# Optimization experiments

Hardware: AMD Instinct MI355X
Metric: run time of the kernel (lower is better)

The kernel has to match this reference:

```python
import jax, jax.numpy as jnp
import numpy as np

N = 50000      # nodes
E = 800000     # edges (avg degree 16)
F_IN = 256
F_OUT = 256


def setup_inputs() -> dict:
    key = jax.random.key(0)
    ks = jax.random.split(key, 8)
    feature = jax.random.normal(ks[0], (N, F_IN), dtype=jnp.float32)
    e_w = jax.random.uniform(ks[1], (E, 1), dtype=jnp.float32)
    snorm_n = jnp.ones((N, 1), dtype=jnp.float32)
    snorm_e = jnp.ones((E, 1), dtype=jnp.float32)
    src = jax.random.randint(ks[2], (E,), 0, N, dtype=jnp.int32)
    dst = jax.random.randint(ks[3], (E,), 0, N, dtype=jnp.int32)
    scale = 1.0 / np.sqrt(F_IN)
    W_self = jax.random.normal(ks[4], (F_IN, F_OUT), dtype=jnp.float32) * scale
    W = jax.random.normal(ks[5], (F_IN, F_OUT), dtype=jnp.float32) * scale
    b = jax.random.normal(ks[6], (F_OUT,), dtype=jnp.float32) * scale
    return {"feature": feature, "e_w": e_w, "snorm_n": snorm_n,
            "snorm_e": snorm_e, "W_self": W_self, "W": W, "b": b,
            "src": src, "dst": dst}


def reference(feature, e_w, snorm_n, snorm_e, W_self, W, b, src, dst):
    n = feature.shape[0]
    ones_e = jnp.ones_like(src, dtype=feature.dtype)
    # self transform
    h_s = feature @ W_self                                   # [N, F_OUT]
    # source-side degree normalization: deg_out^{-1/2}
    out_deg = jnp.maximum(jax.ops.segment_sum(ones_e, src, num_segments=n), 1.0)
    feat = feature * (out_deg ** -0.5)[:, None]              # [N, F_IN]
    # message = h[src] * e_w, aggregated by sum into dst (u_mul_e + sum reduce)
    msgs = feat[src] * e_w                                   # [E, F_IN]
    agg = jax.ops.segment_sum(msgs, dst, num_segments=n)     # [N, F_IN]
    # neighbor transform + destination-side degree normalization
    h = agg @ W + b                                          # [N, F_OUT]
    in_deg = jnp.maximum(jax.ops.segment_sum(ones_e, dst, num_segments=n), 1.0)
    h = h * (in_deg ** -0.5)[:, None]
    return h_s + h, e_w
```

## Files before the change

### kernel.cpp

```cpp
#include <hip/hip_runtime.h>
#include <hip/hip_bf16.h>

#define N_NODES 50000
#define N_EDGES 800000
#define MP      50048
#define MAXDEG  64

#define EDGE_BLOCKS   3125
#define PREP_A_BLOCKS 12512
#define PREPW_BLOCKS  512

typedef __bf16 bf16x8_t __attribute__((ext_vector_type(8)));
typedef float  f32x4_t  __attribute__((ext_vector_type(4)));

__device__ __forceinline__ unsigned short f2bf(float x) {
  __hip_bfloat16 h = __float2bfloat16(x);
  return __builtin_bit_cast(unsigned short, h);
}

__global__ __launch_bounds__(256) void prep_fused(
    const float* __restrict__ feature, const float* __restrict__ Wself,
    const float* __restrict__ W, const float* __restrict__ e_w,
    const int* __restrict__ src, const int* __restrict__ dst,
    unsigned short* __restrict__ Abf, unsigned short* __restrict__ Bt,
    int* __restrict__ cnt_in, int* __restrict__ cnt_out,
    uint2* __restrict__ bucket, float* __restrict__ out1)
{
  const int b = blockIdx.x, tid = threadIdx.x;
  if (b < EDGE_BLOCKS) {
    int e = b * 256 + tid;
    if (e < N_EDGES) {
      int s = src[e];
      int d = dst[e];
      float w = e_w[e];
      out1[e] = w;
      atomicAdd(&cnt_out[s], 1);
      int p = atomicAdd(&cnt_in[d], 1);
      if (p < MAXDEG)
        bucket[(size_t)d * MAXDEG + p] = make_uint2(__float_as_uint(w), (unsigned)s);
    }
  } else if (b < EDGE_BLOCKS + PREP_A_BLOCKS) {
    int idx4 = (b - EDGE_BLOCKS) * 256 + tid;
    size_t base = (size_t)idx4 * 4;
    int row = (int)(base >> 8);
    ushort4 o;
    if (row < N_NODES) {
      const float4 v = *(const float4*)(feature + base);
      o.x = f2bf(v.x); o.y = f2bf(v.y); o.z = f2bf(v.z); o.w = f2bf(v.w);
    } else {
      o.x = o.y = o.z = o.w = 0;
    }
    *(ushort4*)(Abf + base) = o;
  } else {
    int idx = (b - (EDGE_BLOCKS + PREP_A_BLOCKS)) * 256 + tid;
    int n = idx >> 8, k = idx & 255;
    float v = (n < 256) ? Wself[k * 256 + n] : W[k * 256 + (n - 256)];
    Bt[idx] = f2bf(v);
  }
}

__global__ __launch_bounds__(256, 2) void gemm_kernel(
    const unsigned short* __restrict__ A,
    const unsigned short* __restrict__ Bt,
    const float* __restrict__ bias,
    const int* __restrict__ cnt_in,
    const int* __restrict__ cnt_out,
    float* __restrict__ out0,
    unsigned char* __restrict__ y8)
{
  __shared__ unsigned short As[128 * 32];
  __shared__ unsigned short Bs[256 * 32];
  const int tid  = threadIdx.x;
  const int lane = tid & 63;
  const int wave = tid >> 6;
  const int m0 = blockIdx.x * 128;
  const int n0 = blockIdx.y * 256;
  const int wm = (wave & 1) * 64;
  const int wn = (wave >> 1) * 128;
  const int fr = lane & 15;
  const int fk = (lane >> 4) * 8;
  const int srow  = lane >> 2;
  const int scolb = (lane & 3) * 8;

  f32x4_t acc[4][8] = {};

  for (int k0 = 0; k0 < 256; k0 += 32) {
#pragma unroll
    for (int j = 0; j < 2; ++j) {
      int rr = wave * 32 + j * 16;
      const unsigned short* ga = A + (size_t)(m0 + rr + srow) * 256 + (k0 + scolb);
      __builtin_amdgcn_global_load_lds((const __attribute__((address_space(1))) void*)ga,
                                       (__attribute__((address_space(3))) void*)&As[rr * 32],
                                       16, 0, 0);
    }
#pragma unroll
    for (int j = 0; j < 4; ++j) {
      int rr = wave * 64 + j * 16;
      const unsigned short* gb = Bt + (size_t)(n0 + rr + srow) * 256 + (k0 + scolb);
      __builtin_amdgcn_global_load_lds((const __attribute__((address_space(1))) void*)gb,
                                       (__attribute__((address_space(3))) void*)&Bs[rr * 32],
                                       16, 0, 0);
    }
    __syncthreads();

    bf16x8_t af[4], bfr[8];
#pragma unroll
    for (int i = 0; i < 4; ++i)
      af[i]  = *(const bf16x8_t*)&As[(wm + i * 16 + fr) * 32 + fk];
#pragma unroll
    for (int j = 0; j < 8; ++j)
      bfr[j] = *(const bf16x8_t*)&Bs[(wn + j * 16 + fr) * 32 + fk];
#pragma unroll
    for (int i = 0; i < 4; ++i)
#pragma unroll
      for (int j = 0; j < 8; ++j)
        acc[i][j] = __builtin_amdgcn_mfma_f32_16x16x32_bf16(af[i], bfr[j], acc[i][j], 0, 0, 0);
    __syncthreads();
  }

  if (blockIdx.y == 0) {
#pragma unroll
    for (int i = 0; i < 4; ++i) {
      int rowb = m0 + wm + i * 16 + (lane >> 4) * 4;
      float indv[4];
#pragma unroll
      for (int r = 0; r < 4; ++r) {
        int row = rowb + r;
        if (row < N_NODES) {
          int ci = cnt_in[row]; if (ci < 1) ci = 1;
          indv[r] = rsqrtf((float)ci);
        } else indv[r] = 0.f;
      }
#pragma unroll
      for (int j = 0; j < 8; ++j) {
        int col = wn + j * 16 + (lane & 15);
        float bc = bias[col];
#pragma unroll
        for (int r = 0; r < 4; ++r) {
          int row = rowb + r;
          if (row < N_NODES)
            out0[(size_t)row * 256 + col] = acc[i][j][r] + bc * indv[r];
        }
      }
    }
  } else {
#pragma unroll
    for (int i = 0; i < 4; ++i) {
      int rowb = m0 + wm + i * 16 + (lane >> 4) * 4;
      float odv[4];
#pragma unroll
      for (int r = 0; r < 4; ++r) {
        int row = rowb + r;
        if (row < N_NODES) {
          int co = cnt_out[row]; if (co < 1) co = 1;
          odv[r] = rsqrtf((float)co);
        } else odv[r] = 0.f;
      }
#pragma unroll
      for (int j = 0; j < 8; ++j) {
        int col = wn + j * 16 + (lane & 15);
#pragma unroll
        for (int r = 0; r < 4; ++r) {
          int row = rowb + r;
          if (row < N_NODES) {
            float ys = acc[i][j][r] * odv[r];
            unsigned int pk = (unsigned int)__builtin_amdgcn_cvt_pk_fp8_f32(ys, ys, 0, false);
            y8[(size_t)row * 256 + col] = (unsigned char)(pk & 0xffu);
          }
        }
      }
    }
  }
}

__global__ __launch_bounds__(256) void agg_kernel(
    const unsigned char* __restrict__ y8, const uint2* __restrict__ bucket,
    const int* __restrict__ cnt_in, float* __restrict__ out0)
{
  const int wave = threadIdx.x >> 6, lane = threadIdx.x & 63;
  const int node = blockIdx.x * 4 + wave;
  if (node >= N_NODES) return;
  int deg_raw = cnt_in[node];
  int deg = deg_raw > MAXDEG ? MAXDEG : deg_raw;

  uint2 ent = make_uint2(0u, 0u);
  if (lane < deg) ent = bucket[(size_t)node * MAXDEG + lane];
  float wl = __uint_as_float(ent.x);
  int   sl = (int)ent.y;

  float a0 = 0.f, a1 = 0.f, a2 = 0.f, a3 = 0.f;
  for (int b = 0; b < MAXDEG; b += 16) {
    if (b >= deg) break;
#pragma unroll
    for (int t = 0; t < 16; ++t) {
      int eb = b + t;
      int   s = __shfl(sl, eb);
      float w = __shfl(wl, eb);
      bool ok = eb < deg;
      s = ok ? s : 0;
      w = ok ? w : 0.0f;
      unsigned int u = *(const unsigned int*)(y8 + (size_t)s * 256 + lane * 4);
      a0 += w * __builtin_amdgcn_cvt_f32_fp8(u, 0);
      a1 += w * __builtin_amdgcn_cvt_f32_fp8(u, 1);
      a2 += w * __builtin_amdgcn_cvt_f32_fp8(u, 2);
      a3 += w * __builtin_amdgcn_cvt_f32_fp8(u, 3);
    }
  }

  int dn = deg_raw < 1 ? 1 : deg_raw;
  float inv = rsqrtf((float)dn);
  float4 o = *(float4*)(out0 + (size_t)node * 256 + lane * 4);
  o.x += a0 * inv; o.y += a1 * inv; o.z += a2 * inv; o.w += a3 * inv;
  *(float4*)(out0 + (size_t)node * 256 + lane * 4) = o;
}

extern "C" void kernel_launch(void* const* d_in, const int* in_sizes, int n_in,
                              void* d_out, int out_size, void* d_ws, size_t ws_size,
                              hipStream_t stream) {
  const float* feature = (const float*)d_in[0];
  const float* e_w     = (const float*)d_in[1];
  const float* W_self  = (const float*)d_in[4];
  const float* W       = (const float*)d_in[5];
  const float* bias    = (const float*)d_in[6];
  const int*   src     = (const int*)d_in[7];
  const int*   dst     = (const int*)d_in[8];

  float* out0 = (float*)d_out;
  float* out1 = out0 + (size_t)N_NODES * 256;

  char* ws = (char*)d_ws;
  int*            cnt_in  = (int*)(ws + 0);
  int*            cnt_out = (int*)(ws + 204800);
  uint2*          bucket  = (uint2*)(ws + 409600);
  unsigned short* Bt      = (unsigned short*)(ws + 26009600);
  unsigned short* Abf     = (unsigned short*)(ws + 26271744);
  unsigned char*  y8      = (unsigned char*)(ws + 51896320);

  hipMemsetAsync(ws, 0, 409600, stream);

  prep_fused<<<EDGE_BLOCKS + PREP_A_BLOCKS + PREPW_BLOCKS, 256, 0, stream>>>(
      feature, W_self, W, e_w, src, dst, Abf, Bt, cnt_in, cnt_out, bucket, out1);
  gemm_kernel<<<dim3(MP / 128, 2), 256, 0, stream>>>(Abf, Bt, bias, cnt_in, cnt_out, out0, y8);
  agg_kernel<<<(N_NODES + 3) / 4, 256, 0, stream>>>(y8, bucket, cnt_in, out0);
}
```

Before: 283.5 us.

## Pack edge buckets to 32 bits and stage two k-slices per GEMM barrier

Bucket entries now store a bf16 edge weight and a 16-bit source index in one 32-bit word, halving the scatter writes in prep and the bucket reads in aggregation. The GEMM loads two 32-wide k-slices into separate LDS buffers before each barrier, halving the number of synchronisations. Prep block order is changed so the feature conversion blocks are scheduled first. The change relies on node ids fitting in 16 bits, rounds edge weights to bf16, and doubles GEMM LDS usage.

```diff
diff --git a/kernel.cpp b/kernel.cpp
--- a/kernel.cpp
+++ b/kernel.cpp
@@ -6,8 +6,8 @@
 #define MP      50048
 #define MAXDEG  64
 
+#define PREP_A_BLOCKS 12512
 #define EDGE_BLOCKS   3125
-#define PREP_A_BLOCKS 12512
 #define PREPW_BLOCKS  512
 
 typedef __bf16 bf16x8_t __attribute__((ext_vector_type(8)));
@@ -16,6 +16,10 @@
 __device__ __forceinline__ unsigned short f2bf(float x) {
   __hip_bfloat16 h = __float2bfloat16(x);
   return __builtin_bit_cast(unsigned short, h);
+}
+__device__ __forceinline__ float bf2f(unsigned short u) {
+  unsigned int v = ((unsigned int)u) << 16;
+  return __builtin_bit_cast(float, v);
 }
 
 __global__ __launch_bounds__(256) void prep_fused(
@@ -24,23 +28,11 @@
     const int* __restrict__ src, const int* __restrict__ dst,
     unsigned short* __restrict__ Abf, unsigned short* __restrict__ Bt,
     int* __restrict__ cnt_in, int* __restrict__ cnt_out,
-    uint2* __restrict__ bucket, float* __restrict__ out1)
+    unsigned int* __restrict__ bucket, float* __restrict__ out1)
 {
   const int b = blockIdx.x, tid = threadIdx.x;
-  if (b < EDGE_BLOCKS) {
-    int e = b * 256 + tid;
-    if (e < N_EDGES) {
-      int s = src[e];
-      int d = dst[e];
-      float w = e_w[e];
-      out1[e] = w;
-      atomicAdd(&cnt_out[s], 1);
-      int p = atomicAdd(&cnt_in[d], 1);
-      if (p < MAXDEG)
-        bucket[(size_t)d * MAXDEG + p] = make_uint2(__float_as_uint(w), (unsigned)s);
-    }
-  } else if (b < EDGE_BLOCKS + PREP_A_BLOCKS) {
-    int idx4 = (b - EDGE_BLOCKS) * 256 + tid;
+  if (b < PREP_A_BLOCKS) {
+    int idx4 = b * 256 + tid;
     size_t base = (size_t)idx4 * 4;
     int row = (int)(base >> 8);
     ushort4 o;
@@ -51,8 +43,22 @@
       o.x = o.y = o.z = o.w = 0;
     }
     *(ushort4*)(Abf + base) = o;
+  } else if (b < PREP_A_BLOCKS + EDGE_BLOCKS) {
+    int e = (b - PREP_A_BLOCKS) * 256 + tid;
+    if (e < N_EDGES) {
+      int s = src[e];
+      int d = dst[e];
+      float w = e_w[e];
+      out1[e] = w;
+      atomicAdd(&cnt_out[s], 1);
+      int p = atomicAdd(&cnt_in[d], 1);
+      if (p < MAXDEG) {
+        unsigned int ent = ((unsigned int)f2bf(w) << 16) | (unsigned int)s;
+        bucket[(size_t)d * MAXDEG + p] = ent;
+      }
+    }
   } else {
-    int idx = (b - (EDGE_BLOCKS + PREP_A_BLOCKS)) * 256 + tid;
+    int idx = (b - (PREP_A_BLOCKS + EDGE_BLOCKS)) * 256 + tid;
     int n = idx >> 8, k = idx & 255;
     float v = (n < 256) ? Wself[k * 256 + n] : W[k * 256 + (n - 256)];
     Bt[idx] = f2bf(v);
@@ -68,8 +74,8 @@
     float* __restrict__ out0,
     unsigned char* __restrict__ y8)
 {
-  __shared__ unsigned short As[128 * 32];
-  __shared__ unsigned short Bs[256 * 32];
+  __shared__ unsigned short As[2][128 * 32];
+  __shared__ unsigned short Bs[2][256 * 32];
   const int tid  = threadIdx.x;
   const int lane = tid & 63;
   const int wave = tid >> 6;
@@ -84,37 +90,44 @@
 
   f32x4_t acc[4][8] = {};
 
-  for (int k0 = 0; k0 < 256; k0 += 32) {
-#pragma unroll
-    for (int j = 0; j < 2; ++j) {
-      int rr = wave * 32 + j * 16;
-      const unsigned short* ga = A + (size_t)(m0 + rr + srow) * 256 + (k0 + scolb);
-      __builtin_amdgcn_global_load_lds((const __attribute__((address_space(1))) void*)ga,
-                                       (__attribute__((address_space(3))) void*)&As[rr * 32],
-                                       16, 0, 0);
-    }
-#pragma unroll
-    for (int j = 0; j < 4; ++j) {
-      int rr = wave * 64 + j * 16;
-      const unsigned short* gb = Bt + (size_t)(n0 + rr + srow) * 256 + (k0 + scolb);
-      __builtin_amdgcn_global_load_lds((const __attribute__((address_space(1))) void*)gb,
-                                       (__attribute__((address_space(3))) void*)&Bs[rr * 32],
-                                       16, 0, 0);
+  for (int k0 = 0; k0 < 256; k0 += 64) {
+#pragma unroll
+    for (int p = 0; p < 2; ++p) {
+      int kk = k0 + p * 32;
+#pragma unroll
+      for (int j = 0; j < 2; ++j) {
+        int rr = wave * 32 + j * 16;
+        const unsigned short* ga = A + (size_t)(m0 + rr + srow) * 256 + (kk + scolb);
+        __builtin_amdgcn_global_load_lds((const __attribute__((address_space(1))) void*)ga,
+                                         (__attribute__((address_space(3))) void*)&As[p][rr * 32],
+                                         16, 0, 0);
+      }
+#pragma unroll
+      for (int j = 0; j < 4; ++j) {
+        int rr = wave * 64 + j * 16;
+        const unsigned short* gb = Bt + (size_t)(n0 + rr + srow) * 256 + (kk + scolb);
+        __builtin_amdgcn_global_load_lds((const __attribute__((address_space(1))) void*)gb,
+                                         (__attribute__((address_space(3))) void*)&Bs[p][rr * 32],
+                                         16, 0, 0);
+      }
     }
     __syncthreads();
 
-    bf16x8_t af[4], bfr[8];
-#pragma unroll
-    for (int i = 0; i < 4; ++i)
-      af[i]  = *(const bf16x8_t*)&As[(wm + i * 16 + fr) * 32 + fk];
-#pragma unroll
-    for (int j = 0; j < 8; ++j)
-      bfr[j] = *(const bf16x8_t*)&Bs[(wn + j * 16 + fr) * 32 + fk];
-#pragma unroll
-    for (int i = 0; i < 4; ++i)
+#pragma unroll
+    for (int p = 0; p < 2; ++p) {
+      bf16x8_t af[4], bfr[8];
+#pragma unroll
+      for (int i = 0; i < 4; ++i)
+        af[i]  = *(const bf16x8_t*)&As[p][(wm + i * 16 + fr) * 32 + fk];
 #pragma unroll
       for (int j = 0; j < 8; ++j)
-        acc[i][j] = __builtin_amdgcn_mfma_f32_16x16x32_bf16(af[i], bfr[j], acc[i][j], 0, 0, 0);
+        bfr[j] = *(const bf16x8_t*)&Bs[p][(wn + j * 16 + fr) * 32 + fk];
+#pragma unroll
+      for (int i = 0; i < 4; ++i)
+#pragma unroll
+        for (int j = 0; j < 8; ++j)
+          acc[i][j] = __builtin_amdgcn_mfma_f32_16x16x32_bf16(af[i], bfr[j], acc[i][j], 0, 0, 0);
+    }
     __syncthreads();
   }
 
@@ -174,7 +187,7 @@
 }
 
 __global__ __launch_bounds__(256) void agg_kernel(
-    const unsigned char* __restrict__ y8, const uint2* __restrict__ bucket,
+    const unsigned char* __restrict__ y8, const unsigned int* __restrict__ bucket,
     const int* __restrict__ cnt_in, float* __restrict__ out0)
 {
   const int wave = threadIdx.x >> 6, lane = threadIdx.x & 63;
@@ -183,10 +196,10 @@
   int deg_raw = cnt_in[node];
   int deg = deg_raw > MAXDEG ? MAXDEG : deg_raw;
 
-  uint2 ent = make_uint2(0u, 0u);
+  unsigned int ent = 0u;
   if (lane < deg) ent = bucket[(size_t)node * MAXDEG + lane];
-  float wl = __uint_as_float(ent.x);
-  int   sl = (int)ent.y;
+  float wl = bf2f((unsigned short)(ent >> 16));
+  int   sl = (int)(ent & 0xffffu);
 
   float a0 = 0.f, a1 = 0.f, a2 = 0.f, a3 = 0.f;
   for (int b = 0; b < MAXDEG; b += 16) {
@@ -231,14 +244,14 @@
   char* ws = (char*)d_ws;
   int*            cnt_in  = (int*)(ws + 0);
   int*            cnt_out = (int*)(ws + 204800);
-  uint2*          bucket  = (uint2*)(ws + 409600);
-  unsigned short* Bt      = (unsigned short*)(ws + 26009600);
-  unsigned short* Abf     = (unsigned short*)(ws + 26271744);
-  unsigned char*  y8      = (unsigned char*)(ws + 51896320);
+  unsigned int*   bucket  = (unsigned int*)(ws + 409600);
+  unsigned short* Bt      = (unsigned short*)(ws + 13209600);
+  unsigned short* Abf     = (unsigned short*)(ws + 13471744);
+  unsigned char*  y8      = (unsigned char*)(ws + 39096320);
 
   hipMemsetAsync(ws, 0, 409600, stream);
 
-  prep_fused<<<EDGE_BLOCKS + PREP_A_BLOCKS + PREPW_BLOCKS, 256, 0, stream>>>(
+  prep_fused<<<PREP_A_BLOCKS + EDGE_BLOCKS + PREPW_BLOCKS, 256, 0, stream>>>(
       feature, W_self, W, e_w, src, dst, Abf, Bt, cnt_in, cnt_out, bucket, out1);
   gemm_kernel<<<dim3(MP / 128, 2), 256, 0, stream>>>(Abf, Bt, bias, cnt_in, cnt_out, out0, y8);
   agg_kernel<<<(N_NODES + 3) / 4, 256, 0, stream>>>(y8, bucket, cnt_in, out0);
```

Measured after the change: 264.2 us. 6.8% less time.
